# Optimization experiments

Measured on AMD Instinct MI355X. Metric: run time of the kernel, lower is better.

The kernel has to match this reference:

```python
import jax, jax.numpy as jnp
import numpy as np

H = 1024
B = 8
S = 2048

def setup_inputs() -> dict:
    key = jax.random.key(0)
    ks = jax.random.split(key, 16)
    w = lambda k, shp: (jax.random.normal(k, shp, dtype=jnp.float32) * 0.02)
    return {
        "hidden_states": jax.random.normal(ks[0], (B, S, H), dtype=jnp.float32),
        "context_vector": jax.random.normal(ks[1], (B, H), dtype=jnp.float32),
        # nn.Linear weights stored torch-style as [out, in]
        "Wq": w(ks[2], (H, H)), "bq": w(ks[3], (H,)),
        "Wk": w(ks[4], (H, H)), "bk": w(ks[5], (H,)),
        "Wv": w(ks[6], (H, H)), "bv": w(ks[7], (H,)),
        "Wcq": w(ks[8], (H, H)),  # only .weight.t() used in original (no bias)
        "Wck": w(ks[9], (H, H)),
        "g_qh": jax.random.normal(ks[10], (H, 1), dtype=jnp.float32),
        "g_kh": jax.random.normal(ks[11], (H, 1), dtype=jnp.float32),
        "g_qc": jax.random.normal(ks[12], (H, 1), dtype=jnp.float32),
        "g_kc": jax.random.normal(ks[13], (H, 1), dtype=jnp.float32),
    }

def reference(hidden_states, context_vector, Wq, bq, Wk, bk, Wv, bv, Wcq, Wck, g_qh, g_kh, g_qc, g_kc):
    # Linear projections (torch Linear: x @ W.T + b)
    query = jnp.einsum('bsh,oh->bso', hidden_states, Wq) + bq   # [B,S,H]
    key_  = jnp.einsum('bsh,oh->bso', hidden_states, Wk) + bk
    value = jnp.einsum('bsh,oh->bso', hidden_states, Wv) + bv

    # gate = sigmoid(Q @ g_h + (ctx @ g_c)[:,None,:])  -> [B,S,1]
    q_gate = jax.nn.sigmoid(query @ g_qh + (context_vector @ g_qc)[:, None, :])
    k_gate = jax.nn.sigmoid(key_  @ g_kh + (context_vector @ g_kc)[:, None, :])

    # context projections: ctx @ weight.t() (no bias in original usage) -> [B,1,H]
    ctx_q = (context_vector @ Wcq.T)[:, None, :]
    ctx_k = (context_vector @ Wck.T)[:, None, :]

    query_hat = (1.0 - q_gate) * query + q_gate * ctx_q
    key_hat   = (1.0 - k_gate) * key_  + k_gate * ctx_k

    scale = 1.0 / jnp.sqrt(jnp.asarray(H, dtype=jnp.float32))
    scores = jnp.einsum('bqh,bkh->bqk', query_hat, key_hat) * scale  # [B,S,S]
    probs = jax.nn.softmax(scores, axis=-1)
    output = jnp.einsum('bqk,bkh->bqh', probs, value)  # [B,S,H]
    return (output, scores)
```

## Files before the change

kernel.cpp:

```cpp
#include <hip/hip_runtime.h>
#include <cstdint>
#include <cstddef>

#define H 1024
#define NB 8
#define S 2048
#define MROWS (NB*S)

using short8  = __attribute__((ext_vector_type(8))) short;
using ushort8 = __attribute__((ext_vector_type(8))) unsigned short;
using f32x4   = __attribute__((ext_vector_type(4))) float;

__device__ __forceinline__ unsigned short f2bf(float f){
  union { float f; unsigned int u; } c; c.f = f;
  unsigned int u = c.u;
  return (unsigned short)((u + 0x7fffu + ((u >> 16) & 1u)) >> 16);
}


__global__ void k_cvt3(const float* __restrict__ a, const float* __restrict__ b, const float* __restrict__ c,
                       unsigned short* __restrict__ oa, unsigned short* __restrict__ ob, unsigned short* __restrict__ oc){
  const float* src = blockIdx.y == 0 ? a : (blockIdx.y == 1 ? b : c);
  unsigned short* dst = blockIdx.y == 0 ? oa : (blockIdx.y == 1 ? ob : oc);
  int i = (blockIdx.x * 256 + threadIdx.x) * 4;
  float4 v = *reinterpret_cast<const float4*>(src + i);
  ushort4 o;
  o.x = f2bf(v.x); o.y = f2bf(v.y); o.z = f2bf(v.z); o.w = f2bf(v.w);
  *reinterpret_cast<ushort4*>(dst + i) = o;
}

__global__ void k_colproj(const float* __restrict__ Wq_, const float* __restrict__ Wk_,
                          const float* __restrict__ gqh, const float* __restrict__ gkh,
                          float* __restrict__ up){
  const int z = blockIdx.z;
  const float* W = z ? Wk_ : Wq_;
  const float* g = z ? gkh : gqh;
  const int in = blockIdx.x * 256 + threadIdx.x;
  const int o0 = blockIdx.y * 128;
  float s = 0.f;
  for (int o = 0; o < 128; ++o) s = fmaf(W[(size_t)(o0 + o) * H + in], g[o0 + o], s);
  up[(z * 8 + blockIdx.y) * 1024 + in] = s;
}

__global__ void k_ucombine(const float* __restrict__ up, float* __restrict__ u2){
  int i = blockIdx.x * 256 + threadIdx.x;
  int z = i >> 10, h = i & 1023;
  float s = 0.f;
  #pragma unroll
  for (int c = 0; c < 8; ++c) s += up[(z * 8 + c) * 1024 + h];
  u2[i] = s;
}

__global__ __launch_bounds__(256) void k_ctxproj(const float* __restrict__ Wcq, const float* __restrict__ Wck,
    const float* __restrict__ ctx, float* __restrict__ outq, float* __restrict__ outk){
  __shared__ float cs[NB * H];
  const float* W = blockIdx.y ? Wck : Wcq;
  float* out = blockIdx.y ? outk : outq;
  const int t = threadIdx.x;
  for (int i = t; i < NB * H; i += 256) cs[i] = ctx[i];
  __syncthreads();
  const int wid = t >> 6, lane = t & 63;
  const int row = blockIdx.x * 4 + wid;
  float a[NB];
  #pragma unroll
  for (int b = 0; b < NB; ++b) a[b] = 0.f;
  for (int i0 = 0; i0 < H; i0 += 64){
    const float w = W[(size_t)row * H + i0 + lane];
    #pragma unroll
    for (int b = 0; b < NB; ++b) a[b] = fmaf(w, cs[b * H + i0 + lane], a[b]);
  }
  #pragma unroll
  for (int b = 0; b < NB; ++b){
    float v = a[b];
    #pragma unroll
    for (int off = 32; off > 0; off >>= 1) v += __shfl_xor(v, off);
    if (lane == 0) out[b * H + row] = v;
  }
}

__global__ __launch_bounds__(512) void k_scalars(const float* __restrict__ bq, const float* __restrict__ gqh,
    const float* __restrict__ bk, const float* __restrict__ gkh,
    const float* __restrict__ ctx, const float* __restrict__ gqc, const float* __restrict__ gkc,
    float* __restrict__ scal){
  const int wid = threadIdx.x >> 6, lane = threadIdx.x & 63;
  for (int d = wid; d < 18; d += 8){
    const float *pa, *pb;
    if (d == 0){ pa = bq; pb = gqh; }
    else if (d == 1){ pa = bk; pb = gkh; }
    else if (d < 10){ pa = ctx + (d - 2) * H; pb = gqc; }
    else { pa = ctx + (d - 10) * H; pb = gkc; }
    float s = 0.f;
    for (int i = lane; i < H; i += 64) s = fmaf(pa[i], pb[i], s);
    #pragma unroll
    for (int off = 32; off > 0; off >>= 1) s += __shfl_xor(s, off);
    if (lane == 0) scal[d] = s;
  }
}

__global__ __launch_bounds__(256) void k_prepass(const float* __restrict__ hs,
    const float* __restrict__ u2, const float* __restrict__ scal,
    unsigned short* __restrict__ hsb, float* __restrict__ gq, float* __restrict__ gk){
  const int t = threadIdx.x, wid = t >> 6, lane = t & 63;
  const int row = blockIdx.x * 4 + wid;
  const float* hrow = hs + (size_t)row * H;
  const float* u_q = u2;
  const float* u_k = u2 + 1024;
  unsigned short* orow = hsb + (size_t)row * H;
  float sq = 0.f, sk = 0.f;
  #pragma unroll
  for (int c = 0; c < 4; ++c){
    const int idx = (lane + c * 64) * 4;
    float4 v  = *reinterpret_cast<const float4*>(hrow + idx);
    float4 uq = *reinterpret_cast<const float4*>(u_q + idx);
    float4 uk = *reinterpret_cast<const float4*>(u_k + idx);
    ushort4 o; o.x = f2bf(v.x); o.y = f2bf(v.y); o.z = f2bf(v.z); o.w = f2bf(v.w);
    *reinterpret_cast<ushort4*>(orow + idx) = o;
    sq += v.x*uq.x + v.y*uq.y + v.z*uq.z + v.w*uq.w;
    sk += v.x*uk.x + v.y*uk.y + v.z*uk.z + v.w*uk.w;
  }
  #pragma unroll
  for (int off = 32; off > 0; off >>= 1){
    sq += __shfl_xor(sq, off);
    sk += __shfl_xor(sk, off);
  }
  if (lane == 0){
    const int b = row >> 11;
    gq[row] = 1.f / (1.f + __expf(-(sq + scal[0] + scal[2 + b])));
    gk[row] = 1.f / (1.f + __expf(-(sk + scal[1] + scal[10 + b])));
  }
}


#define STG(bufi, opi, halfi, koff, P0, P1) \
  do { __builtin_amdgcn_global_load_lds((const __attribute__((address_space(1))) void*)(P0 + (koff)), \
      (__attribute__((address_space(3))) void*)((char*)(&lds[bufi][opi][halfi][0]) + (wid*2+0)*1024), 16, 0, 0); \
    __builtin_amdgcn_global_load_lds((const __attribute__((address_space(1))) void*)(P1 + (koff)), \
      (__attribute__((address_space(3))) void*)((char*)(&lds[bufi][opi][halfi][0]) + (wid*2+1)*1024), 16, 0, 0); } while(0)
#define STG_A(bufi, halfi, koff) STG(bufi, 0, halfi, koff, sA0, sA1)
#define STG_B(bufi, halfi, koff) STG(bufi, 1, halfi, koff, sB0, sB1)

#define DS_A(bufi, ks, mh) \
  do { _Pragma("unroll") for (int m_ = 0; m_ < 4; ++m_){ \
      const int ar_ = wr*128 + ((mh)*4 + m_)*16 + (lane & 15); \
      const int sl_ = (lane >> 4) ^ ((ar_ >> 1) & 3); \
      af[m_] = *reinterpret_cast<const short8*>(&lds[bufi][0][ks][ar_*32 + sl_*8]); } } while(0)
#define DS_B(bufi, ks) \
  do { _Pragma("unroll") for (int n_ = 0; n_ < 4; ++n_){ \
      const int br_ = wc*64 + n_*16 + (lane & 15); \
      const int sl_ = (lane >> 4) ^ ((br_ >> 1) & 3); \
      bf[n_] = *reinterpret_cast<const short8*>(&lds[bufi][1][ks][br_*32 + sl_*8]); } } while(0)
#define MFMA16(mh) \
  do { __builtin_amdgcn_s_setprio(1); \
    _Pragma("unroll") for (int m_ = 0; m_ < 4; ++m_) \
      _Pragma("unroll") for (int n_ = 0; n_ < 4; ++n_) \
        acc[(mh)*4 + m_][n_] = __builtin_amdgcn_mfma_f32_16x16x32_bf16(af[m_], bf[n_], acc[(mh)*4 + m_][n_], 0, 0, 0); \
    __builtin_amdgcn_s_setprio(0); } while(0)
#define VM4() do { asm volatile("s_waitcnt vmcnt(4)" ::: "memory"); } while(0)
#define VM0() do { asm volatile("s_waitcnt vmcnt(0)" ::: "memory"); } while(0)
#define BAR() do { asm volatile("" ::: "memory"); __builtin_amdgcn_s_barrier(); asm volatile("" ::: "memory"); } while(0)

template<int MODE>
__global__ __launch_bounds__(512, 2)
void k_gemm(const unsigned short* __restrict__ A, const unsigned short* __restrict__ B,
            int K, int ldA, int ldB, long long Abatch, long long Bbatch,
            const float* __restrict__ gate, const float* __restrict__ bias,
            const float* __restrict__ ctxv,
            unsigned short* __restrict__ outb, float* __restrict__ outf,
            long long outBatch, float scale)
{
  __shared__ __align__(16) short lds[2][2][2][8192];

  const int t = threadIdx.x;
  const int wid = t >> 6, lane = t & 63;
  const int wr = wid >> 2, wc = wid & 3;
  const int bz = blockIdx.z;
  const unsigned short* Ab = A + (size_t)bz * (size_t)Abatch;
  const unsigned short* Bb = B + (size_t)bz * (size_t)Bbatch;
  const int row0 = blockIdx.x * 256;
  const int col0 = blockIdx.y * 256;

  const int c0 = (wid*2 + 0)*64 + lane;
  const int c1 = (wid*2 + 1)*64 + lane;
  const int r0s = c0 >> 2, r1s = c1 >> 2;
  const int kc0 = (c0 & 3) ^ ((r0s >> 1) & 3);
  const int kc1 = (c1 & 3) ^ ((r1s >> 1) & 3);
  const unsigned short* sA0 = Ab + (size_t)(row0 + r0s) * (size_t)ldA + kc0*8;
  const unsigned short* sA1 = Ab + (size_t)(row0 + r1s) * (size_t)ldA + kc1*8;
  const unsigned short* sB0 = Bb + (size_t)(col0 + r0s) * (size_t)ldB + kc0*8;
  const unsigned short* sB1 = Bb + (size_t)(col0 + r1s) * (size_t)ldB + kc1*8;

  f32x4 acc[8][4] = {};
  short8 af[4], bf[4];

  STG_A(0, 0, 0); STG_B(0, 0, 0); STG_A(0, 1, 32); STG_B(0, 1, 32);
  VM0(); BAR();

  const int niter = K >> 7;
  for (int it = 0; it < niter; ++it){
    const int t1k = (it*2 + 1) << 6;
    const int t2k = (it*2 + 2) << 6;
    const bool more = (it + 1 < niter);
    DS_A(0, 0, 0); DS_B(0, 0); STG_A(1, 0, t1k);      MFMA16(0);                              BAR();
    DS_A(0, 0, 1);             STG_B(1, 0, t1k);      MFMA16(1); VM4();                       BAR();
    DS_A(0, 1, 0); DS_B(0, 1); STG_A(1, 1, t1k + 32); MFMA16(0);                              BAR();
    DS_A(0, 1, 1);             STG_B(1, 1, t1k + 32); MFMA16(1); if (more) { VM4(); } else { VM0(); } BAR();
    DS_A(1, 0, 0); DS_B(1, 0); if (more) { STG_A(0, 0, t2k); }      MFMA16(0);                BAR();
    DS_A(1, 0, 1);             if (more) { STG_B(0, 0, t2k); }      MFMA16(1); if (more) { VM4(); } BAR();
    DS_A(1, 1, 0); DS_B(1, 1); if (more) { STG_A(0, 1, t2k + 32); } MFMA16(0);                BAR();
    DS_A(1, 1, 1);             if (more) { STG_B(0, 1, t2k + 32); } MFMA16(1); if (more) { VM4(); } BAR();
  }

  if constexpr (MODE == 0){
    unsigned short* tp = (unsigned short*)lds;
    float* gl = (float*)((char*)lds + 69632);
    float* bl = gl + 256;
    float* cl = bl + 256;
    const int b = row0 >> 11;
    __syncthreads();
    if (t < 256){
      gl[t] = gate[row0 + t];
      bl[t] = bias[col0 + t];
      cl[t] = ctxv[b * H + col0 + t];
    }
    __syncthreads();
    #pragma unroll
    for (int ci = 0; ci < 2; ++ci){
      if (ci) __syncthreads();
      if (wr == ci){
        #pragma unroll
        for (int mi = 0; mi < 8; ++mi)
          #pragma unroll
          for (int r = 0; r < 4; ++r){
            const int lr = mi*16 + (lane >> 4)*4 + r;
            const float g = gl[ci*128 + lr];
            #pragma unroll
            for (int n = 0; n < 4; ++n){
              const int lc = wc*64 + n*16 + (lane & 15);
              const float q = acc[mi][n][r] + bl[lc];
              tp[lr*264 + lc] = f2bf((1.f - g) * q + g * cl[lc]);
            }
          }
      }
      __syncthreads();
      const int rr = t & 127;
      const int cc = (t >> 7) * 64;
      const unsigned short* srcp = tp + rr*264 + cc;
      unsigned short* dst = outb + (size_t)(row0 + ci*128 + rr) * H + col0 + cc;
      #pragma unroll
      for (int i = 0; i < 64; i += 8)
        *reinterpret_cast<ushort8*>(dst + i) = *reinterpret_cast<const ushort8*>(srcp + i);
    }
  } else if constexpr (MODE == 2){
    unsigned short* tp = (unsigned short*)lds;
    const int bb = row0 >> 11;
    const int s0 = row0 & (S - 1);
    #pragma unroll
    for (int ci = 0; ci < 2; ++ci)
      #pragma unroll
      for (int cj = 0; cj < 2; ++cj){
        __syncthreads();
        if (wr == ci && (wc >> 1) == cj){
          const int lc0 = (wc & 1) * 64;
          #pragma unroll
          for (int mi = 0; mi < 8; ++mi)
            #pragma unroll
            for (int n = 0; n < 4; ++n)
              #pragma unroll
              for (int r = 0; r < 4; ++r){
                const int lr = mi*16 + (lane >> 4)*4 + r;
                const int lc = lc0 + n*16 + (lane & 15);
                tp[lc*136 + lr] = f2bf(acc[mi][n][r] + bias[col0 + cj*128 + lc]);
              }
        }
        __syncthreads();
        const int hh = t & 127;
        const int sc = (t >> 7) * 32;
        const unsigned short* srcp = tp + hh*136 + sc;
        unsigned short* vout = outb + (size_t)bb * H * S + (size_t)(col0 + cj*128 + hh) * S
                                    + (size_t)(s0 + ci*128 + sc);
        #pragma unroll
        for (int i2 = 0; i2 < 32; i2 += 8)
          *reinterpret_cast<ushort8*>(vout + i2) = *reinterpret_cast<const ushort8*>(srcp + i2);
      }
  } else if constexpr (MODE == 3){
    #pragma unroll
    for (int mi = 0; mi < 8; ++mi)
      #pragma unroll
      for (int n = 0; n < 4; ++n)
        #pragma unroll
        for (int r = 0; r < 4; ++r){
          const int grow = row0 + wr*128 + mi*16 + (lane >> 4)*4 + r;
          const int gcol = col0 + wc*64 + n*16 + (lane & 15);
          outf[(size_t)bz * (size_t)outBatch + (size_t)grow * S + gcol] = acc[mi][n][r] * scale;
        }
  } else {
    #pragma unroll
    for (int mi = 0; mi < 8; ++mi)
      #pragma unroll
      for (int n = 0; n < 4; ++n)
        #pragma unroll
        for (int r = 0; r < 4; ++r){
          const int grow = row0 + wr*128 + mi*16 + (lane >> 4)*4 + r;
          const int gcol = col0 + wc*64 + n*16 + (lane & 15);
          outf[(size_t)bz * (size_t)outBatch + (size_t)grow * H + gcol] = acc[mi][n][r];
        }
  }
}

__global__ __launch_bounds__(256) void k_softmax(const float* __restrict__ scores,
                                                 unsigned short* __restrict__ probs){
  const int row = blockIdx.x;
  const float* srow = scores + (size_t)row * S;
  unsigned short* prow = probs + (size_t)row * S;
  const int t = threadIdx.x, wid = t >> 6, lane = t & 63;
  __shared__ float red[8];
  float4 v0 = *reinterpret_cast<const float4*>(srow + t * 4);
  float4 v1 = *reinterpret_cast<const float4*>(srow + 1024 + t * 4);
  float m = fmaxf(fmaxf(fmaxf(v0.x, v0.y), fmaxf(v0.z, v0.w)),
                  fmaxf(fmaxf(v1.x, v1.y), fmaxf(v1.z, v1.w)));
  #pragma unroll
  for (int off = 32; off > 0; off >>= 1) m = fmaxf(m, __shfl_xor(m, off));
  if (lane == 0) red[wid] = m;
  __syncthreads();
  m = fmaxf(fmaxf(red[0], red[1]), fmaxf(red[2], red[3]));
  float4 e0, e1;
  e0.x = __expf(v0.x - m); e0.y = __expf(v0.y - m); e0.z = __expf(v0.z - m); e0.w = __expf(v0.w - m);
  e1.x = __expf(v1.x - m); e1.y = __expf(v1.y - m); e1.z = __expf(v1.z - m); e1.w = __expf(v1.w - m);
  float s = (e0.x + e0.y + e0.z + e0.w) + (e1.x + e1.y + e1.z + e1.w);
  #pragma unroll
  for (int off = 32; off > 0; off >>= 1) s += __shfl_xor(s, off);
  if (lane == 0) red[4 + wid] = s;
  __syncthreads();
  s = (red[4] + red[5]) + (red[6] + red[7]);
  const float inv = 1.f / s;
  ushort4 o;
  o.x = f2bf(e0.x * inv); o.y = f2bf(e0.y * inv); o.z = f2bf(e0.z * inv); o.w = f2bf(e0.w * inv);
  *reinterpret_cast<ushort4*>(prow + t * 4) = o;
  o.x = f2bf(e1.x * inv); o.y = f2bf(e1.y * inv); o.z = f2bf(e1.z * inv); o.w = f2bf(e1.w * inv);
  *reinterpret_cast<ushort4*>(prow + 1024 + t * 4) = o;
}

extern "C" void kernel_launch(void* const* d_in, const int* in_sizes, int n_in,
                              void* d_out, int out_size, void* d_ws, size_t ws_size,
                              hipStream_t stream) {
  const float* hs  = (const float*)d_in[0];
  const float* ctx = (const float*)d_in[1];
  const float* Wq  = (const float*)d_in[2];
  const float* bq  = (const float*)d_in[3];
  const float* Wk  = (const float*)d_in[4];
  const float* bk  = (const float*)d_in[5];
  const float* Wv  = (const float*)d_in[6];
  const float* bv  = (const float*)d_in[7];
  const float* Wcq = (const float*)d_in[8];
  const float* Wck = (const float*)d_in[9];
  const float* gqh = (const float*)d_in[10];
  const float* gkh = (const float*)d_in[11];
  const float* gqc = (const float*)d_in[12];
  const float* gkc = (const float*)d_in[13];

  char* ws = (char*)d_ws;
  unsigned short* hsb   = (unsigned short*)(ws);
  unsigned short* qhat  = (unsigned short*)(ws + 33554432);
  unsigned short* khat  = (unsigned short*)(ws + 67108864);
  unsigned short* vt    = (unsigned short*)(ws + 100663296);
  unsigned short* probs = (unsigned short*)(ws + 134217728);
  unsigned short* wqb   = (unsigned short*)(ws + 167772160);
  unsigned short* wkb   = (unsigned short*)(ws + 169869312);
  unsigned short* wvb   = (unsigned short*)(ws + 171966464);
  float* up    = (float*)(ws + 174063616);
  float* u2    = (float*)(ws + 174129152);
  float* ctxq  = (float*)(ws + 174137344);
  float* ctxk  = (float*)(ws + 174170112);
  float* gq    = (float*)(ws + 174202880);
  float* gk    = (float*)(ws + 174268416);
  float* scal  = (float*)(ws + 174333952);

  float* out_attn   = (float*)d_out;
  float* out_scores = out_attn + (size_t)MROWS * H;

  k_cvt3<<<dim3(1024, 3), 256, 0, stream>>>(Wq, Wk, Wv, wqb, wkb, wvb);
  k_colproj<<<dim3(4, 8, 2), 256, 0, stream>>>(Wq, Wk, gqh, gkh, up);
  k_ucombine<<<8, 256, 0, stream>>>(up, u2);
  k_ctxproj<<<dim3(256, 2), 256, 0, stream>>>(Wcq, Wck, ctx, ctxq, ctxk);
  k_scalars<<<1, 512, 0, stream>>>(bq, gqh, bk, gkh, ctx, gqc, gkc, scal);
  k_prepass<<<MROWS / 4, 256, 0, stream>>>(hs, u2, scal, hsb, gq, gk);

  k_gemm<0><<<dim3(64, 4, 1), 512, 0, stream>>>(hsb, wqb, 1024, 1024, 1024, 0, 0,
      gq, bq, ctxq, qhat, nullptr, 0, 1.f);
  k_gemm<0><<<dim3(64, 4, 1), 512, 0, stream>>>(hsb, wkb, 1024, 1024, 1024, 0, 0,
      gk, bk, ctxk, khat, nullptr, 0, 1.f);

  k_gemm<2><<<dim3(64, 4, 1), 512, 0, stream>>>(hsb, wvb, 1024, 1024, 1024, 0, 0,
      nullptr, bv, nullptr, vt, nullptr, 0, 1.f);

  k_gemm<3><<<dim3(8, 8, 8), 512, 0, stream>>>(qhat, khat, 1024, 1024, 1024,
      (long long)S * H, (long long)S * H, nullptr, nullptr, nullptr,
      nullptr, out_scores, (long long)S * S, 0.03125f);

  k_softmax<<<MROWS, 256, 0, stream>>>(out_scores, probs);

  k_gemm<4><<<dim3(8, 4, 8), 512, 0, stream>>>(probs, vt, 2048, 2048, 2048,
      (long long)S * S, (long long)H * S, nullptr, nullptr, nullptr,
      nullptr, out_attn, (long long)S * H, 1.f);
}
```

Before: 362.8 us.

## Merge small prep kernels and fuse Q/K/V projection GEMMs into one launch

Four small setup kernels (weight bf16 conversion, gate column projection, context projections, scalar dot products) become one kernel that branches on block index. The three Q/K/V projection GEMMs become a single 64x12 grid. Each block picks its epilogue (gated Q/K or transposed V) from its column offset, relying on the three bf16 weight matrices sitting back to back in the workspace. This cuts launch overhead and fills the GPU with a larger grid to reduce tail idling, at the cost of more branching and parameters in the GEMM epilogue.

Measured after the change: 338.8 us. 1.07x faster.

```diff
diff --git a/kernel.cpp b/kernel.cpp
--- a/kernel.cpp
+++ b/kernel.cpp
@@ -17,29 +17,80 @@
   return (unsigned short)((u + 0x7fffu + ((u >> 16) & 1u)) >> 16);
 }
 
-
-__global__ void k_cvt3(const float* __restrict__ a, const float* __restrict__ b, const float* __restrict__ c,
-                       unsigned short* __restrict__ oa, unsigned short* __restrict__ ob, unsigned short* __restrict__ oc){
-  const float* src = blockIdx.y == 0 ? a : (blockIdx.y == 1 ? b : c);
-  unsigned short* dst = blockIdx.y == 0 ? oa : (blockIdx.y == 1 ? ob : oc);
-  int i = (blockIdx.x * 256 + threadIdx.x) * 4;
-  float4 v = *reinterpret_cast<const float4*>(src + i);
-  ushort4 o;
-  o.x = f2bf(v.x); o.y = f2bf(v.y); o.z = f2bf(v.z); o.w = f2bf(v.w);
-  *reinterpret_cast<ushort4*>(dst + i) = o;
-}
-
-__global__ void k_colproj(const float* __restrict__ Wq_, const float* __restrict__ Wk_,
-                          const float* __restrict__ gqh, const float* __restrict__ gkh,
-                          float* __restrict__ up){
-  const int z = blockIdx.z;
-  const float* W = z ? Wk_ : Wq_;
-  const float* g = z ? gkh : gqh;
-  const int in = blockIdx.x * 256 + threadIdx.x;
-  const int o0 = blockIdx.y * 128;
-  float s = 0.f;
-  for (int o = 0; o < 128; ++o) s = fmaf(W[(size_t)(o0 + o) * H + in], g[o0 + o], s);
-  up[(z * 8 + blockIdx.y) * 1024 + in] = s;
+__global__ __launch_bounds__(256) void k_prep(
+    const float* __restrict__ Wq, const float* __restrict__ Wk, const float* __restrict__ Wv,
+    const float* __restrict__ Wcq, const float* __restrict__ Wck, const float* __restrict__ ctx,
+    const float* __restrict__ gqh, const float* __restrict__ gkh,
+    const float* __restrict__ bq, const float* __restrict__ bk,
+    const float* __restrict__ gqc, const float* __restrict__ gkc,
+    unsigned short* __restrict__ wqb, unsigned short* __restrict__ wkb, unsigned short* __restrict__ wvb,
+    float* __restrict__ up, float* __restrict__ ctxq, float* __restrict__ ctxk,
+    float* __restrict__ scal)
+{
+  __shared__ float cs[NB * H];
+  const int bid = blockIdx.x;
+  const int t = threadIdx.x;
+  if (bid < 3072){
+    const int y = bid >> 10;
+    const int x = bid & 1023;
+    const float* src = y == 0 ? Wq : (y == 1 ? Wk : Wv);
+    unsigned short* dst = y == 0 ? wqb : (y == 1 ? wkb : wvb);
+    const int i = (x * 256 + t) * 4;
+    float4 v = *reinterpret_cast<const float4*>(src + i);
+    ushort4 o; o.x = f2bf(v.x); o.y = f2bf(v.y); o.z = f2bf(v.z); o.w = f2bf(v.w);
+    *reinterpret_cast<ushort4*>(dst + i) = o;
+  } else if (bid < 3136){
+    const int sub = bid - 3072;
+    const int z = sub >> 5;
+    const int y = (sub >> 2) & 7;
+    const int x = sub & 3;
+    const float* W = z ? Wk : Wq;
+    const float* g = z ? gkh : gqh;
+    const int in = x * 256 + t;
+    const int o0 = y * 128;
+    float s = 0.f;
+    for (int o = 0; o < 128; ++o) s = fmaf(W[(size_t)(o0 + o) * H + in], g[o0 + o], s);
+    up[(z * 8 + y) * 1024 + in] = s;
+  } else if (bid < 3648){
+    const int sub = bid - 3136;
+    const int y = sub >> 8;
+    const int x = sub & 255;
+    const float* W = y ? Wck : Wcq;
+    float* out = y ? ctxk : ctxq;
+    for (int i = t; i < NB * H; i += 256) cs[i] = ctx[i];
+    __syncthreads();
+    const int wid = t >> 6, lane = t & 63;
+    const int row = x * 4 + wid;
+    float a[NB];
+    #pragma unroll
+    for (int b = 0; b < NB; ++b) a[b] = 0.f;
+    for (int i0 = 0; i0 < H; i0 += 64){
+      const float w = W[(size_t)row * H + i0 + lane];
+      #pragma unroll
+      for (int b = 0; b < NB; ++b) a[b] = fmaf(w, cs[b * H + i0 + lane], a[b]);
+    }
+    #pragma unroll
+    for (int b = 0; b < NB; ++b){
+      float v = a[b];
+      #pragma unroll
+      for (int off = 32; off > 0; off >>= 1) v += __shfl_xor(v, off);
+      if (lane == 0) out[b * H + row] = v;
+    }
+  } else {
+    const int wid = t >> 6, lane = t & 63;
+    for (int d = wid; d < 18; d += 4){
+      const float *pa, *pb;
+      if (d == 0){ pa = bq; pb = gqh; }
+      else if (d == 1){ pa = bk; pb = gkh; }
+      else if (d < 10){ pa = ctx + (d - 2) * H; pb = gqc; }
+      else { pa = ctx + (d - 10) * H; pb = gkc; }
+      float s = 0.f;
+      for (int i = lane; i < H; i += 64) s = fmaf(pa[i], pb[i], s);
+      #pragma unroll
+      for (int off = 32; off > 0; off >>= 1) s += __shfl_xor(s, off);
+      if (lane == 0) scal[d] = s;
+    }
+  }
 }
 
 __global__ void k_ucombine(const float* __restrict__ up, float* __restrict__ u2){
@@ -49,52 +100,6 @@
   #pragma unroll
   for (int c = 0; c < 8; ++c) s += up[(z * 8 + c) * 1024 + h];
   u2[i] = s;
-}
-
-__global__ __launch_bounds__(256) void k_ctxproj(const float* __restrict__ Wcq, const float* __restrict__ Wck,
-    const float* __restrict__ ctx, float* __restrict__ outq, float* __restrict__ outk){
-  __shared__ float cs[NB * H];
-  const float* W = blockIdx.y ? Wck : Wcq;
-  float* out = blockIdx.y ? outk : outq;
-  const int t = threadIdx.x;
-  for (int i = t; i < NB * H; i += 256) cs[i] = ctx[i];
-  __syncthreads();
-  const int wid = t >> 6, lane = t & 63;
-  const int row = blockIdx.x * 4 + wid;
-  float a[NB];
-  #pragma unroll
-  for (int b = 0; b < NB; ++b) a[b] = 0.f;
-  for (int i0 = 0; i0 < H; i0 += 64){
-    const float w = W[(size_t)row * H + i0 + lane];
-    #pragma unroll
-    for (int b = 0; b < NB; ++b) a[b] = fmaf(w, cs[b * H + i0 + lane], a[b]);
-  }
-  #pragma unroll
-  for (int b = 0; b < NB; ++b){
-    float v = a[b];
-    #pragma unroll
-    for (int off = 32; off > 0; off >>= 1) v += __shfl_xor(v, off);
-    if (lane == 0) out[b * H + row] = v;
-  }
-}
-
-__global__ __launch_bounds__(512) void k_scalars(const float* __restrict__ bq, const float* __restrict__ gqh,
-    const float* __restrict__ bk, const float* __restrict__ gkh,
-    const float* __restrict__ ctx, const float* __restrict__ gqc, const float* __restrict__ gkc,
-    float* __restrict__ scal){
-  const int wid = threadIdx.x >> 6, lane = threadIdx.x & 63;
-  for (int d = wid; d < 18; d += 8){
-    const float *pa, *pb;
-    if (d == 0){ pa = bq; pb = gqh; }
-    else if (d == 1){ pa = bk; pb = gkh; }
-    else if (d < 10){ pa = ctx + (d - 2) * H; pb = gqc; }
-    else { pa = ctx + (d - 10) * H; pb = gkc; }
-    float s = 0.f;
-    for (int i = lane; i < H; i += 64) s = fmaf(pa[i], pb[i], s);
-    #pragma unroll
-    for (int off = 32; off > 0; off >>= 1) s += __shfl_xor(s, off);
-    if (lane == 0) scal[d] = s;
-  }
 }
 
 __global__ __launch_bounds__(256) void k_prepass(const float* __restrict__ hs,
@@ -163,10 +168,11 @@
 __global__ __launch_bounds__(512, 2)
 void k_gemm(const unsigned short* __restrict__ A, const unsigned short* __restrict__ B,
             int K, int ldA, int ldB, long long Abatch, long long Bbatch,
-            const float* __restrict__ gate, const float* __restrict__ bias,
-            const float* __restrict__ ctxv,
-            unsigned short* __restrict__ outb, float* __restrict__ outf,
-            long long outBatch, float scale)
+            const float* __restrict__ gq, const float* __restrict__ gk,
+            const float* __restrict__ bq, const float* __restrict__ bk, const float* __restrict__ bv,
+            const float* __restrict__ cq, const float* __restrict__ ck,
+            unsigned short* __restrict__ oq, unsigned short* __restrict__ ok, unsigned short* __restrict__ ov,
+            float* __restrict__ outf, long long outBatch, float scale)
 {
   __shared__ __align__(16) short lds[2][2][2][8192];
 
@@ -211,77 +217,85 @@
   }
 
   if constexpr (MODE == 0){
-    unsigned short* tp = (unsigned short*)lds;
-    float* gl = (float*)((char*)lds + 69632);
-    float* bl = gl + 256;
-    float* cl = bl + 256;
-    const int b = row0 >> 11;
-    __syncthreads();
-    if (t < 256){
-      gl[t] = gate[row0 + t];
-      bl[t] = bias[col0 + t];
-      cl[t] = ctxv[b * H + col0 + t];
-    }
-    __syncthreads();
-    #pragma unroll
-    for (int ci = 0; ci < 2; ++ci){
-      if (ci) __syncthreads();
-      if (wr == ci){
-        #pragma unroll
-        for (int mi = 0; mi < 8; ++mi)
-          #pragma unroll
-          for (int r = 0; r < 4; ++r){
-            const int lr = mi*16 + (lane >> 4)*4 + r;
-            const float g = gl[ci*128 + lr];
-            #pragma unroll
-            for (int n = 0; n < 4; ++n){
-              const int lc = wc*64 + n*16 + (lane & 15);
-              const float q = acc[mi][n][r] + bl[lc];
-              tp[lr*264 + lc] = f2bf((1.f - g) * q + g * cl[lc]);
-            }
-          }
+    const int which = col0 >> 10;
+    const int lcol  = col0 & 1023;
+    if (which < 2){
+      const float* gate = which ? gk : gq;
+      const float* bias = which ? bk : bq;
+      const float* ctxv = which ? ck : cq;
+      unsigned short* outb = which ? ok : oq;
+      unsigned short* tp = (unsigned short*)lds;
+      float* gl = (float*)((char*)lds + 69632);
+      float* bl = gl + 256;
+      float* cl = bl + 256;
+      const int b = row0 >> 11;
+      __syncthreads();
+      if (t < 256){
+        gl[t] = gate[row0 + t];
+        bl[t] = bias[lcol + t];
+        cl[t] = ctxv[b * H + lcol + t];
       }
       __syncthreads();
-      const int rr = t & 127;
-      const int cc = (t >> 7) * 64;
-      const unsigned short* srcp = tp + rr*264 + cc;
-      unsigned short* dst = outb + (size_t)(row0 + ci*128 + rr) * H + col0 + cc;
-      #pragma unroll
-      for (int i = 0; i < 64; i += 8)
-        *reinterpret_cast<ushort8*>(dst + i) = *reinterpret_cast<const ushort8*>(srcp + i);
-    }
-  } else if constexpr (MODE == 2){
-    unsigned short* tp = (unsigned short*)lds;
-    const int bb = row0 >> 11;
-    const int s0 = row0 & (S - 1);
-    #pragma unroll
-    for (int ci = 0; ci < 2; ++ci)
-      #pragma unroll
-      for (int cj = 0; cj < 2; ++cj){
-        __syncthreads();
-        if (wr == ci && (wc >> 1) == cj){
-          const int lc0 = (wc & 1) * 64;
+      #pragma unroll
+      for (int ci = 0; ci < 2; ++ci){
+        if (ci) __syncthreads();
+        if (wr == ci){
           #pragma unroll
           for (int mi = 0; mi < 8; ++mi)
             #pragma unroll
-            for (int n = 0; n < 4; ++n)
+            for (int r = 0; r < 4; ++r){
+              const int lr = mi*16 + (lane >> 4)*4 + r;
+              const float g = gl[ci*128 + lr];
               #pragma unroll
-              for (int r = 0; r < 4; ++r){
-                const int lr = mi*16 + (lane >> 4)*4 + r;
-                const int lc = lc0 + n*16 + (lane & 15);
-                tp[lc*136 + lr] = f2bf(acc[mi][n][r] + bias[col0 + cj*128 + lc]);
+              for (int n = 0; n < 4; ++n){
+                const int lc = wc*64 + n*16 + (lane & 15);
+                const float q = acc[mi][n][r] + bl[lc];
+                tp[lr*264 + lc] = f2bf((1.f - g) * q + g * cl[lc]);
               }
+            }
         }
         __syncthreads();
-        const int hh = t & 127;
-        const int sc = (t >> 7) * 32;
-        const unsigned short* srcp = tp + hh*136 + sc;
-        unsigned short* vout = outb + (size_t)bb * H * S + (size_t)(col0 + cj*128 + hh) * S
+        const int rr = t & 127;
+        const int cc = (t >> 7) * 64;
+        const unsigned short* srcp = tp + rr*264 + cc;
+        unsigned short* dst = outb + (size_t)(row0 + ci*128 + rr) * H + lcol + cc;
+        #pragma unroll
+        for (int i = 0; i < 64; i += 8)
+          *reinterpret_cast<ushort8*>(dst + i) = *reinterpret_cast<const ushort8*>(srcp + i);
+      }
+    } else {
+      unsigned short* tp = (unsigned short*)lds;
+      const int bb = row0 >> 11;
+      const int s0 = row0 & (S - 1);
+      #pragma unroll
+      for (int ci = 0; ci < 2; ++ci)
+        #pragma unroll
+        for (int cj = 0; cj < 2; ++cj){
+          __syncthreads();
+          if (wr == ci && (wc >> 1) == cj){
+            const int lc0 = (wc & 1) * 64;
+            #pragma unroll
+            for (int mi = 0; mi < 8; ++mi)
+              #pragma unroll
+              for (int n = 0; n < 4; ++n)
+                #pragma unroll
+                for (int r = 0; r < 4; ++r){
+                  const int lr = mi*16 + (lane >> 4)*4 + r;
+                  const int lc = lc0 + n*16 + (lane & 15);
+                  tp[lc*136 + lr] = f2bf(acc[mi][n][r] + bv[lcol + cj*128 + lc]);
+                }
+          }
+          __syncthreads();
+          const int hh = t & 127;
+          const int sc = (t >> 7) * 32;
+          const unsigned short* srcp = tp + hh*136 + sc;
+          unsigned short* vout = ov + (size_t)bb * H * S + (size_t)(lcol + cj*128 + hh) * S
                                     + (size_t)(s0 + ci*128 + sc);
-        #pragma unroll
-        for (int i2 = 0; i2 < 32; i2 += 8)
-          *reinterpret_cast<ushort8*>(vout + i2) = *reinterpret_cast<const ushort8*>(srcp + i2);
-      }
+          #pragma unroll
+          for (int i2 = 0; i2 < 32; i2 += 8)
+            *reinterpret_cast<ushort8*>(vout + i2) = *reinterpret_cast<const ushort8*>(srcp + i2);
+        }
+    }
   } else if constexpr (MODE == 3){
     #pragma unroll
     for (int mi = 0; mi < 8; ++mi)
@@ -378,28 +392,23 @@
   float* out_attn   = (float*)d_out;
   float* out_scores = out_attn + (size_t)MROWS * H;
 
-  k_cvt3<<<dim3(1024, 3), 256, 0, stream>>>(Wq, Wk, Wv, wqb, wkb, wvb);
-  k_colproj<<<dim3(4, 8, 2), 256, 0, stream>>>(Wq, Wk, gqh, gkh, up);
+  k_prep<<<3649, 256, 0, stream>>>(Wq, Wk, Wv, Wcq, Wck, ctx, gqh, gkh, bq, bk, gqc, gkc,
+      wqb, wkb, wvb, up, ctxq, ctxk, scal);
   k_ucombine<<<8, 256, 0, stream>>>(up, u2);
-  k_ctxproj<<<dim3(256, 2), 256, 0, stream>>>(Wcq, Wck, ctx, ctxq, ctxk);
-  k_scalars<<<1, 512, 0, stream>>>(bq, gqh, bk, gkh, ctx, gqc, gkc, scal);
   k_prepass<<<MROWS / 4, 256, 0, stream>>>(hs, u2, scal, hsb, gq, gk);
 
-  k_gemm<0><<<dim3(64, 4, 1), 512, 0, stream>>>(hsb, wqb, 1024, 1024, 1024, 0, 0,
-      gq, bq, ctxq, qhat, nullptr, 0, 1.f);
-  k_gemm<0><<<dim3(64, 4, 1), 512, 0, stream>>>(hsb, wkb, 1024, 1024, 1024, 0, 0,
-      gk, bk, ctxk, khat, nullptr, 0, 1.f);
-
-  k_gemm<2><<<dim3(64, 4, 1), 512, 0, stream>>>(hsb, wvb, 1024, 1024, 1024, 0, 0,
-      nullptr, bv, nullptr, vt, nullptr, 0, 1.f);
+  k_gemm<0><<<dim3(64, 12, 1), 512, 0, stream>>>(hsb, wqb, 1024, 1024, 1024, 0, 0,
+      gq, gk, bq, bk, bv, ctxq, ctxk, qhat, khat, vt, nullptr, 0, 1.f);
 
   k_gemm<3><<<dim3(8, 8, 8), 512, 0, stream>>>(qhat, khat, 1024, 1024, 1024,
-      (long long)S * H, (long long)S * H, nullptr, nullptr, nullptr,
-      nullptr, out_scores, (long long)S * S, 0.03125f);
+      (long long)S * H, (long long)S * H,
+      nullptr, nullptr, nullptr, nullptr, nullptr, nullptr, nullptr,
+      nullptr, nullptr, nullptr, out_scores, (long long)S * S, 0.03125f);
 
   k_softmax<<<MROWS, 256, 0, stream>>>(out_scores, probs);
 
   k_gemm<4><<<dim3(8, 4, 8), 512, 0, stream>>>(probs, vt, 2048, 2048, 2048,
-      (long long)S * S, (long long)H * S, nullptr, nullptr, nullptr,
-      nullptr, out_attn, (long long)S * H, 1.f);
-}
+      (long long)S * S, (long long)H * S,
+      nullptr, nullptr, nullptr, nullptr, nullptr, nullptr, nullptr,
+      nullptr, nullptr, nullptr, out_attn, (long long)S * H, 1.f);
+}
```
